# Kernel tuning notes

Hardware: AMD Instinct MI355X
Metric: run time of the kernel (lower is better)

The kernel has to match this reference:

```python
import jax, jax.numpy as jnp
import numpy as np

N_AE = 512
N_DE = 256
N = 100000
NUM_SEG = 1024
EPS = 1e-5


def setup_inputs() -> dict:
    key = jax.random.key(0)
    ks = jax.random.split(key, 20)
    d_in1 = 2 * N_AE + N_DE  # 1280
    inp = {
        "x": jax.random.normal(ks[0], (N, 2 * N_AE), dtype=jnp.float32),
        "dist_feat": jax.random.normal(ks[1], (N, N_DE), dtype=jnp.float32),
        "atom_idx": jax.random.randint(ks[2], (N,), 0, 100, dtype=jnp.int32),
        "ele_idx": jax.random.randint(ks[3], (N,), 0, NUM_SEG, dtype=jnp.int32),
        # layer 1 params
        "l1_w": jax.random.normal(ks[4], (d_in1, N_AE), dtype=jnp.float32) * (1.0 / np.sqrt(d_in1)),
        "l1_b": jnp.zeros((N_AE,), dtype=jnp.float32),
        "l1_g": jnp.ones((N_AE,), dtype=jnp.float32),
        "l1_be": jnp.zeros((N_AE,), dtype=jnp.float32),
        # layer 2 params (same input width: 2*n_ae + n_de)
        "l2_w": jax.random.normal(ks[5], (d_in1, N_AE), dtype=jnp.float32) * (1.0 / np.sqrt(d_in1)),
        "l2_b": jnp.zeros((N_AE,), dtype=jnp.float32),
        "l2_g": jnp.ones((N_AE,), dtype=jnp.float32),
        "l2_be": jnp.zeros((N_AE,), dtype=jnp.float32),
        # final fc + bn
        "f_w": jax.random.normal(ks[6], (2 * N_AE, N_AE), dtype=jnp.float32) * (1.0 / np.sqrt(2 * N_AE)),
        "f_b": jnp.zeros((N_AE,), dtype=jnp.float32),
        "f_g": jnp.ones((N_AE,), dtype=jnp.float32),
        "f_be": jnp.zeros((N_AE,), dtype=jnp.float32),
    }
    return inp


def _bn(h, gamma, beta):
    # BatchNorm1d in training mode: batch stats, biased variance
    m = jnp.mean(h, axis=0)
    v = jnp.mean(jnp.square(h - m), axis=0)
    return gamma * (h - m) * jax.lax.rsqrt(v + EPS) + beta


def _dist_layer(x_cat, ele_idx, w, b, gamma, beta):
    h = jax.nn.relu(_bn(x_cat @ w + b, gamma, beta))  # [N, n_ae]
    sums = jax.ops.segment_sum(h, ele_idx, num_segments=NUM_SEG)  # [S, n_ae]
    cnt = jax.ops.segment_sum(jnp.ones((h.shape[0],), h.dtype), ele_idx, num_segments=NUM_SEG)
    mean = sums / jnp.maximum(cnt, 1.0)[:, None]
    return jnp.concatenate([h, mean[ele_idx]], axis=1)  # [N, 2*n_ae]


def reference(x, dist_feat, atom_idx, ele_idx,
              l1_w, l1_b, l1_g, l1_be,
              l2_w, l2_b, l2_g, l2_be,
              f_w, f_b, f_g, f_be):
    h = _dist_layer(jnp.concatenate([x, dist_feat], axis=1), ele_idx, l1_w, l1_b, l1_g, l1_be)
    h = _dist_layer(jnp.concatenate([h, dist_feat], axis=1), ele_idx, l2_w, l2_b, l2_g, l2_be)
    out = jax.nn.relu(_bn(h @ f_w + f_b, f_g, f_be))  # [N, n_ae]
    return out
```

## Files before the change

kernel.cpp:

```cpp
#include <hip/hip_runtime.h>
#include <stdint.h>
#include <stdio.h>

#define NOUT 512
#define NSEG 1024

typedef unsigned short u16;
typedef __attribute__((ext_vector_type(4))) float f32x4;
typedef __attribute__((ext_vector_type(8))) short s16x8;
typedef __attribute__((ext_vector_type(4))) unsigned short u16x4;

__device__ __forceinline__ u16 f2b(float f) {
  union { float f; uint32_t u; } v; v.f = f;
  uint32_t r = v.u + 0x7FFFu + ((v.u >> 16) & 1u);
  return (u16)(r >> 16);
}
__device__ __forceinline__ float b2f(u16 b) {
  union { uint32_t u; float f; } v; v.u = ((uint32_t)b) << 16;
  return v.f;
}

typedef __attribute__((address_space(1))) const void GAS;
typedef __attribute__((address_space(3))) void LAS;
__device__ __forceinline__ void llds16(const void* g, void* l) {
  __builtin_amdgcn_global_load_lds((GAS*)g, (LAS*)l, 16, 0, 0);
}

__global__ void k_cast2(const float* __restrict__ x, u16* __restrict__ xb, long n4x,
                        const float* __restrict__ d, u16* __restrict__ db, long n4d) {
  long i0 = blockIdx.x * (long)blockDim.x + threadIdx.x;
  long stride = (long)gridDim.x * blockDim.x;
  for (long i = i0; i < n4x; i += stride) {
    float4 v = reinterpret_cast<const float4*>(x)[i];
    u16x4 o;
    o.x = f2b(v.x); o.y = f2b(v.y); o.z = f2b(v.z); o.w = f2b(v.w);
    reinterpret_cast<u16x4*>(xb)[i] = o;
  }
  for (long i = i0; i < n4d; i += stride) {
    float4 v = reinterpret_cast<const float4*>(d)[i];
    u16x4 o;
    o.x = f2b(v.x); o.y = f2b(v.y); o.z = f2b(v.z); o.w = f2b(v.w);
    reinterpret_cast<u16x4*>(db)[i] = o;
  }
}

__global__ void k_wtcastT3(const float* __restrict__ w0, u16* __restrict__ o0,
                           const float* __restrict__ w1, u16* __restrict__ o1,
                           const float* __restrict__ w2, u16* __restrict__ o2) {
  __shared__ float tile[32][33];
  int z = blockIdx.z;
  const float* w = z == 0 ? w0 : (z == 1 ? w1 : w2);
  u16* out = z == 0 ? o0 : (z == 1 ? o1 : o2);
  int K = z == 2 ? 1024 : 1280;
  int k0 = blockIdx.x * 32, c0 = blockIdx.y * 32;
  if (k0 >= K) return;
  int t = threadIdx.x;
  int rr = t >> 5, cc = t & 31;
#pragma unroll
  for (int p = 0; p < 4; ++p)
    tile[p * 8 + rr][cc] = w[(long)(k0 + p * 8 + rr) * NOUT + c0 + cc];
  __syncthreads();
#pragma unroll
  for (int p = 0; p < 4; ++p)
    out[(long)(c0 + p * 8 + rr) * K + k0 + cc] = f2b(tile[cc][p * 8 + rr]);
}

__global__ void k_hist(const int* __restrict__ ele, int* __restrict__ cnt, int N) {
  int i = blockIdx.x * blockDim.x + threadIdx.x;
  int stride = gridDim.x * blockDim.x;
  for (; i < N; i += stride) atomicAdd(&cnt[ele[i]], 1);
}

__global__ void k_scan(const int* __restrict__ cnt, int* __restrict__ off) {
  __shared__ int tmp[NSEG];
  int t = threadIdx.x;
  tmp[t] = cnt[t];
  __syncthreads();
  for (int o = 1; o < NSEG; o <<= 1) {
    int add = (t >= o) ? tmp[t - o] : 0;
    __syncthreads();
    tmp[t] += add;
    __syncthreads();
  }
  off[t] = tmp[t] - cnt[t];
}

__global__ void k_scatter(const int* __restrict__ ele, const int* __restrict__ off,
                          int* __restrict__ fill, int* __restrict__ rows, int N) {
  int i = blockIdx.x * blockDim.x + threadIdx.x;
  int stride = gridDim.x * blockDim.x;
  for (; i < N; i += stride) {
    int e = ele[i];
    int p = atomicAdd(&fill[e], 1);
    rows[off[e] + p] = i;
  }
}

__global__ void k_bnseg(const u16* __restrict__ hp, u16* __restrict__ h, u16* __restrict__ mean,
                        const float* __restrict__ stats, const float* __restrict__ g,
                        const float* __restrict__ be, float invM,
                        const int* __restrict__ off, const int* __restrict__ cnt,
                        const int* __restrict__ rows) {
  int s = blockIdx.x;
  int c0 = 2 * threadIdx.x;
  int n = cnt[s], o = off[s];
  float m0 = stats[c0] * invM, m1 = stats[c0 + 1] * invM;
  float v0 = stats[NOUT + c0] * invM - m0 * m0;
  float v1 = stats[NOUT + c0 + 1] * invM - m1 * m1;
  float a0 = g[c0] * rsqrtf(v0 + 1e-5f);
  float a1 = g[c0 + 1] * rsqrtf(v1 + 1e-5f);
  float cc0 = be[c0] - a0 * m0;
  float cc1 = be[c0 + 1] - a1 * m1;
  float s0 = 0.f, s1 = 0.f;
#pragma unroll 2
  for (int j = 0; j < n; ++j) {
    int r = rows[o + j];
    uint32_t v = *reinterpret_cast<const uint32_t*>(&hp[(long)r * NOUT + c0]);
    float h0 = fmaxf(a0 * b2f((u16)(v & 0xffff)) + cc0, 0.f);
    float h1 = fmaxf(a1 * b2f((u16)(v >> 16)) + cc1, 0.f);
    s0 += h0; s1 += h1;
    *reinterpret_cast<uint32_t*>(&h[(long)r * NOUT + c0]) =
        ((uint32_t)f2b(h1) << 16) | (uint32_t)f2b(h0);
  }
  float inv = 1.f / fmaxf((float)n, 1.f);
  *reinterpret_cast<uint32_t*>(&mean[(long)s * NOUT + c0]) =
      ((uint32_t)f2b(s1 * inv) << 16) | (uint32_t)f2b(s0 * inv);
}

__global__ void k_final(const u16* __restrict__ hp, float* __restrict__ out,
                        const float* __restrict__ stats, const float* __restrict__ g,
                        const float* __restrict__ be, float invM, long n4) {
  __shared__ float sA[NOUT], sC[NOUT];
  for (int c = threadIdx.x; c < NOUT; c += blockDim.x) {
    float m = stats[c] * invM;
    float v = stats[NOUT + c] * invM - m * m;
    float a = g[c] * rsqrtf(v + 1e-5f);
    sA[c] = a;
    sC[c] = be[c] - a * m;
  }
  __syncthreads();
  long i = blockIdx.x * (long)blockDim.x + threadIdx.x;
  long stride = (long)gridDim.x * blockDim.x;
  for (; i < n4; i += stride) {
    u16x4 v = reinterpret_cast<const u16x4*>(hp)[i];
    int c0 = (int)((i * 4) & (NOUT - 1));
    float4 a = *reinterpret_cast<const float4*>(&sA[c0]);
    float4 c = *reinterpret_cast<const float4*>(&sC[c0]);
    float4 o;
    o.x = fmaxf(a.x * b2f(v.x) + c.x, 0.f);
    o.y = fmaxf(a.y * b2f(v.y) + c.y, 0.f);
    o.z = fmaxf(a.z * b2f(v.z) + c.z, 0.f);
    o.w = fmaxf(a.w * b2f(v.w) + c.w, 0.f);
    reinterpret_cast<float4*>(out)[i] = o;
  }
}

template <int K, int E0, int E0B, int BSKIP>
__global__ __launch_bounds__(256, 4) void k_gemm(
    const u16* p0, const u16* p1, int w0, int w1, int g0, int g1,
    const int* __restrict__ ele,
    const u16* __restrict__ wbt, int ldb,
    const float* __restrict__ tab, int addtab,
    u16* __restrict__ outp, float* __restrict__ outf, int wf32,
    float* __restrict__ csum, float* __restrict__ csq, int dostats,
    int M) {
  __shared__ __align__(16) u16 As[2 * 4096];
  __shared__ __align__(16) u16 Bs[2 * 4096];

  int nwg = gridDim.x;
  int orig = blockIdx.x;
  int q = nwg >> 3, r8 = nwg & 7;
  int xcd = orig & 7, loc = orig >> 3;
  int bid = (xcd < r8 ? xcd * (q + 1) : r8 * (q + 1) + (xcd - r8) * q) + loc;
  int mt = bid >> 2, ct = bid & 3;
  int brow = mt * 128, bcol = ct * 128;

  int tid = (int)threadIdx.x;
  int lane = tid & 63;
  int wid = tid >> 6;
  int wr = wid >> 1, wc = wid & 1;
  int l15 = lane & 15, kg = lane >> 4;

  int srow = tid >> 2;
  int soct = ((tid & 3) ^ ((srow >> 1) & 3)) * 8;

  int gr0 = brow + srow, gr1 = gr0 + 64;
  int gr0c = gr0 < M ? gr0 : M - 1;
  int gr1c = gr1 < M ? gr1 : M - 1;
  int el0 = (g0 | g1) ? ele[gr0c] : 0, el1 = (g0 | g1) ? ele[gr1c] : 0;

  const u16* a00 = p0 + (long)(g0 ? el0 : gr0c) * w0 + soct;
  const u16* a01 = p1 + (long)(g1 ? el0 : gr0c) * w1 + soct - E0;
  const u16* a10 = p0 + (long)(g0 ? el1 : gr1c) * w0 + soct;
  const u16* a11 = p1 + (long)(g1 ? el1 : gr1c) * w1 + soct - E0;

  const u16* b0p = wbt + (long)(bcol + srow) * ldb + soct;
  const u16* b1p = wbt + (long)(bcol + srow + 64) * ldb + soct;

  int xoct = (kg ^ ((l15 >> 1) & 3)) * 8;
  int aro = (wr * 64 + l15) * 32 + xoct;
  int bro = (wc * 64 + l15) * 32 + xoct;

  f32x4 acc[4][4];
#pragma unroll
  for (int m = 0; m < 4; ++m)
#pragma unroll
    for (int n = 0; n < 4; ++n)
#pragma unroll
      for (int j = 0; j < 4; ++j) acc[m][n][j] = 0.f;

  constexpr int KT = K >> 5;
  int dst = wid * 512;

  auto stage = [&](int tt, int buf) {
    int k0 = tt << 5;
    const u16* sa0 = k0 < E0 ? a00 : a01;
    const u16* sa1 = k0 < E0 ? a10 : a11;
    int bo = k0 + (k0 >= E0B ? BSKIP : 0);
    int ab = buf * 4096 + dst;
    llds16(sa0 + k0, &As[ab]);
    llds16(sa1 + k0, &As[ab + 2048]);
    llds16(b0p + bo, &Bs[ab]);
    llds16(b1p + bo, &Bs[ab + 2048]);
  };

  stage(0, 0);
  __syncthreads();

#pragma unroll
  for (int t = 0; t < KT; ++t) {
    int cur = t & 1;
    if (t + 1 < KT) stage(t + 1, cur ^ 1);
    __builtin_amdgcn_sched_barrier(0);
    const u16* Ab = &As[cur * 4096];
    const u16* Bb = &Bs[cur * 4096];
    s16x8 af[4], bf[4];
#pragma unroll
    for (int m = 0; m < 4; ++m)
      af[m] = *reinterpret_cast<const s16x8*>(&Ab[m * 512 + aro]);
#pragma unroll
    for (int n = 0; n < 4; ++n)
      bf[n] = *reinterpret_cast<const s16x8*>(&Bb[n * 512 + bro]);
#pragma unroll
    for (int m = 0; m < 4; ++m)
#pragma unroll
      for (int n = 0; n < 4; ++n)
        acc[m][n] = __builtin_amdgcn_mfma_f32_16x16x32_bf16(af[m], bf[n], acc[m][n], 0, 0, 0);
    __syncthreads();
  }

  float sums[4] = {0.f, 0.f, 0.f, 0.f}, sqs[4] = {0.f, 0.f, 0.f, 0.f};
#pragma unroll
  for (int m = 0; m < 4; ++m) {
    int row0 = brow + wr * 64 + m * 16 + kg * 4;
#pragma unroll
    for (int j = 0; j < 4; ++j) {
      int r = row0 + j;
      if (r < M) {
        long rb = (long)r * NOUT;
        long tb = addtab ? (long)ele[r] * NOUT : 0;
#pragma unroll
        for (int n = 0; n < 4; ++n) {
          int col = bcol + wc * 64 + n * 16 + l15;
          float v = acc[m][n][j];
          if (addtab) v += tab[tb + col];
          if (wf32) outf[rb + col] = v;
          else outp[rb + col] = f2b(v);
          sums[n] += v;
          sqs[n] += v * v;
        }
      }
    }
  }
  if (dostats) {
#pragma unroll
    for (int n = 0; n < 4; ++n) {
      sums[n] += __shfl_xor(sums[n], 16);
      sums[n] += __shfl_xor(sums[n], 32);
      sqs[n] += __shfl_xor(sqs[n], 16);
      sqs[n] += __shfl_xor(sqs[n], 32);
    }
    if (kg == 0) {
#pragma unroll
      for (int n = 0; n < 4; ++n) {
        int col = bcol + wc * 64 + n * 16 + l15;
        atomicAdd(&csum[col], sums[n]);
        atomicAdd(&csq[col], sqs[n]);
      }
    }
  }
}

extern "C" void kernel_launch(void* const* d_in, const int* in_sizes, int n_in,
                              void* d_out, int out_size, void* d_ws, size_t ws_size,
                              hipStream_t stream) {
  const float* x    = (const float*)d_in[0];
  const float* dist = (const float*)d_in[1];
  const int* ele    = (const int*)d_in[3];
  const float* l1w  = (const float*)d_in[4];
  const float* l1g  = (const float*)d_in[6];
  const float* l1be = (const float*)d_in[7];
  const float* l2w  = (const float*)d_in[8];
  const float* l2g  = (const float*)d_in[10];
  const float* l2be = (const float*)d_in[11];
  const float* fw   = (const float*)d_in[12];
  const float* fg   = (const float*)d_in[14];
  const float* fbe  = (const float*)d_in[15];

  int N = in_sizes[0] / 1024;
  float* out = (float*)d_out;
  u16* xbf = (u16*)d_out;

  int MT = (N + 127) / 128;

  char* w = (char*)d_ws;
  auto alloc = [&](size_t bytes) {
    char* p = w;
    w += (bytes + 255) & ~(size_t)255;
    return p;
  };
  u16* dist_bf = (u16*)alloc((size_t)N * 256 * 2);
  u16* hp      = (u16*)alloc((size_t)N * NOUT * 2);
  u16* h       = (u16*)alloc((size_t)N * NOUT * 2);
  u16* mean    = (u16*)alloc((size_t)NSEG * NOUT * 2);
  u16* w1bt    = (u16*)alloc((size_t)NOUT * 1280 * 2);
  u16* w2bt    = (u16*)alloc((size_t)NOUT * 1280 * 2);
  u16* fbt     = (u16*)alloc((size_t)NOUT * 1024 * 2);
  float* mc2   = (float*)alloc((size_t)NSEG * NOUT * 4);
  float* mc3   = (float*)alloc((size_t)NSEG * NOUT * 4);
  char* zz0    = w;
  int* seg_cnt = (int*)alloc(NSEG * 4);
  int* seg_fill = (int*)alloc(NSEG * 4);
  float* stats1 = (float*)alloc(NOUT * 2 * 4);
  float* stats2 = (float*)alloc(NOUT * 2 * 4);
  float* stats3 = (float*)alloc(NOUT * 2 * 4);
  size_t zzlen = (size_t)(w - zz0);
  int* seg_off = (int*)alloc(NSEG * 4);
  int* rows    = (int*)alloc((size_t)N * 4);

  size_t need = (size_t)(w - (char*)d_ws);
  if (need > ws_size) {
    fprintf(stderr, "kernel_launch: ws too small: need %zu have %zu\n", need, ws_size);
    return;
  }

  long n4x = (long)N * 1024 / 4;
  long n4d = (long)N * 256 / 4;
  long n4h = (long)N * NOUT / 4;
  int gemmGrid = MT * 4;
  int mcGrid = (NSEG / 128) * 4;
  float invM = 1.0f / (float)N;

  k_cast2<<<4096, 256, 0, stream>>>(x, xbf, n4x, dist, dist_bf, n4d);
  dim3 wtg(1280 / 32, NOUT / 32, 3);
  k_wtcastT3<<<wtg, 256, 0, stream>>>(l1w, w1bt, l2w, w2bt, fw, fbt);
  hipMemsetAsync(zz0, 0, zzlen, stream);

  k_hist<<<512, 256, 0, stream>>>(ele, seg_cnt, N);
  k_scan<<<1, NSEG, 0, stream>>>(seg_cnt, seg_off);
  k_scatter<<<512, 256, 0, stream>>>(ele, seg_off, seg_fill, rows, N);

  k_gemm<1280, 1024, 1280, 0><<<gemmGrid, 256, 0, stream>>>(
      xbf, dist_bf, 1024, 256, 0, 0, ele, w1bt, 1280, mc2, 0,
      hp, mc2, 0, stats1, stats1 + NOUT, 1, N);
  k_bnseg<<<NSEG, 256, 0, stream>>>(hp, h, mean, stats1, l1g, l1be, invM,
                                    seg_off, seg_cnt, rows);

  k_gemm<512, 512, 512, 0><<<mcGrid, 256, 0, stream>>>(
      mean, mean, 512, 512, 0, 0, ele, w2bt + 512, 1280, mc2, 0,
      hp, mc2, 1, stats2, stats2 + NOUT, 0, NSEG);
  k_gemm<768, 512, 512, 512><<<gemmGrid, 256, 0, stream>>>(
      h, dist_bf, 512, 256, 0, 0, ele, w2bt, 1280, mc2, 1,
      hp, mc2, 0, stats2, stats2 + NOUT, 1, N);
  k_bnseg<<<NSEG, 256, 0, stream>>>(hp, h, mean, stats2, l2g, l2be, invM,
                                    seg_off, seg_cnt, rows);

  k_gemm<512, 512, 512, 0><<<mcGrid, 256, 0, stream>>>(
      mean, mean, 512, 512, 0, 0, ele, fbt + 512, 1024, mc3, 0,
      hp, mc3, 1, stats3, stats3 + NOUT, 0, NSEG);
  k_gemm<512, 512, 512, 0><<<gemmGrid, 256, 0, stream>>>(
      h, h, 512, 512, 0, 0, ele, fbt, 1024, mc3, 1,
      hp, mc3, 0, stats3, stats3 + NOUT, 1, N);
  k_final<<<4096, 256, 0, stream>>>(hp, out, stats3, fg, fbe, invM, n4h);
}
```

Measured before the change: 908.6 us.

## Enlarge GEMM row tile from 128 to 192 with per-wave loading

The GEMM block tile grows from 128x128 to 192x128, so each wave computes a 96x64 sub-tile with 6x4 MFMA accumulators. Global-to-LDS staging is reorganised so each wave loads three A row-groups and two B row-groups, and the launch bound is lowered to 3 blocks per CU to make room for the extra registers and LDS. The aim is more reuse of each B fragment per LDS load and fewer blocks overall. The cost is lower occupancy, more register pressure, and more wasted rows on the small 1024-row mean GEMM.

Result: slower. 1.023 ms (+12.6%).

```diff
diff --git a/kernel.cpp b/kernel.cpp
--- a/kernel.cpp
+++ b/kernel.cpp
@@ -156,7 +156,7 @@
 }
 
 template <int K, int E0, int E0B, int BSKIP>
-__global__ __launch_bounds__(256, 4) void k_gemm(
+__global__ __launch_bounds__(256, 3) void k_gemm(
     const u16* p0, const u16* p1, int w0, int w1, int g0, int g1,
     const int* __restrict__ ele,
     const u16* __restrict__ wbt, int ldb,
@@ -164,7 +164,7 @@
     u16* __restrict__ outp, float* __restrict__ outf, int wf32,
     float* __restrict__ csum, float* __restrict__ csq, int dostats,
     int M) {
-  __shared__ __align__(16) u16 As[2 * 4096];
+  __shared__ __align__(16) u16 As[2 * 6144];
   __shared__ __align__(16) u16 Bs[2 * 4096];
 
   int nwg = gridDim.x;
@@ -173,7 +173,7 @@
   int xcd = orig & 7, loc = orig >> 3;
   int bid = (xcd < r8 ? xcd * (q + 1) : r8 * (q + 1) + (xcd - r8) * q) + loc;
   int mt = bid >> 2, ct = bid & 3;
-  int brow = mt * 128, bcol = ct * 128;
+  int brow = mt * 192, bcol = ct * 128;
 
   int tid = (int)threadIdx.x;
   int lane = tid & 63;
@@ -181,47 +181,52 @@
   int wr = wid >> 1, wc = wid & 1;
   int l15 = lane & 15, kg = lane >> 4;
 
-  int srow = tid >> 2;
-  int soct = ((tid & 3) ^ ((srow >> 1) & 3)) * 8;
-
-  int gr0 = brow + srow, gr1 = gr0 + 64;
-  int gr0c = gr0 < M ? gr0 : M - 1;
-  int gr1c = gr1 < M ? gr1 : M - 1;
-  int el0 = (g0 | g1) ? ele[gr0c] : 0, el1 = (g0 | g1) ? ele[gr1c] : 0;
-
-  const u16* a00 = p0 + (long)(g0 ? el0 : gr0c) * w0 + soct;
-  const u16* a01 = p1 + (long)(g1 ? el0 : gr0c) * w1 + soct - E0;
-  const u16* a10 = p0 + (long)(g0 ? el1 : gr1c) * w0 + soct;
-  const u16* a11 = p1 + (long)(g1 ? el1 : gr1c) * w1 + soct - E0;
-
-  const u16* b0p = wbt + (long)(bcol + srow) * ldb + soct;
-  const u16* b1p = wbt + (long)(bcol + srow + 64) * ldb + soct;
+  int lrow = lane >> 2;
+  int lsoct = ((lane & 3) ^ ((lane >> 3) & 3)) * 8;
+
+  const u16 *a0p[3], *a1p[3];
+#pragma unroll
+  for (int i = 0; i < 3; ++i) {
+    int gr = brow + 16 * (wid * 3 + i) + lrow;
+    if (gr >= M) gr = M - 1;
+    int e = (g0 | g1) ? ele[gr] : 0;
+    a0p[i] = p0 + (long)(g0 ? e : gr) * w0 + lsoct;
+    a1p[i] = p1 + (long)(g1 ? e : gr) * w1 + lsoct - E0;
+  }
+  const u16* bp[2];
+#pragma unroll
+  for (int i = 0; i < 2; ++i)
+    bp[i] = wbt + (long)(bcol + 16 * (wid * 2 + i) + lrow) * ldb + lsoct;
 
   int xoct = (kg ^ ((l15 >> 1) & 3)) * 8;
-  int aro = (wr * 64 + l15) * 32 + xoct;
+  int aro = (wr * 96 + l15) * 32 + xoct;
   int bro = (wc * 64 + l15) * 32 + xoct;
 
-  f32x4 acc[4][4];
-#pragma unroll
-  for (int m = 0; m < 4; ++m)
+  f32x4 acc[6][4];
+#pragma unroll
+  for (int m = 0; m < 6; ++m)
 #pragma unroll
     for (int n = 0; n < 4; ++n)
 #pragma unroll
       for (int j = 0; j < 4; ++j) acc[m][n][j] = 0.f;
 
   constexpr int KT = K >> 5;
-  int dst = wid * 512;
 
   auto stage = [&](int tt, int buf) {
     int k0 = tt << 5;
-    const u16* sa0 = k0 < E0 ? a00 : a01;
-    const u16* sa1 = k0 < E0 ? a10 : a11;
     int bo = k0 + (k0 >= E0B ? BSKIP : 0);
-    int ab = buf * 4096 + dst;
-    llds16(sa0 + k0, &As[ab]);
-    llds16(sa1 + k0, &As[ab + 2048]);
-    llds16(b0p + bo, &Bs[ab]);
-    llds16(b1p + bo, &Bs[ab + 2048]);
+    if (k0 < E0) {
+#pragma unroll
+      for (int i = 0; i < 3; ++i)
+        llds16(a0p[i] + k0, &As[buf * 6144 + (wid * 3 + i) * 512]);
+    } else {
+#pragma unroll
+      for (int i = 0; i < 3; ++i)
+        llds16(a1p[i] + k0, &As[buf * 6144 + (wid * 3 + i) * 512]);
+    }
+#pragma unroll
+    for (int i = 0; i < 2; ++i)
+      llds16(bp[i] + bo, &Bs[buf * 4096 + (wid * 2 + i) * 512]);
   };
 
   stage(0, 0);
@@ -232,17 +237,17 @@
     int cur = t & 1;
     if (t + 1 < KT) stage(t + 1, cur ^ 1);
     __builtin_amdgcn_sched_barrier(0);
-    const u16* Ab = &As[cur * 4096];
+    const u16* Ab = &As[cur * 6144];
     const u16* Bb = &Bs[cur * 4096];
-    s16x8 af[4], bf[4];
-#pragma unroll
-    for (int m = 0; m < 4; ++m)
+    s16x8 af[6], bf[4];
+#pragma unroll
+    for (int m = 0; m < 6; ++m)
       af[m] = *reinterpret_cast<const s16x8*>(&Ab[m * 512 + aro]);
 #pragma unroll
     for (int n = 0; n < 4; ++n)
       bf[n] = *reinterpret_cast<const s16x8*>(&Bb[n * 512 + bro]);
 #pragma unroll
-    for (int m = 0; m < 4; ++m)
+    for (int m = 0; m < 6; ++m)
 #pragma unroll
       for (int n = 0; n < 4; ++n)
         acc[m][n] = __builtin_amdgcn_mfma_f32_16x16x32_bf16(af[m], bf[n], acc[m][n], 0, 0, 0);
@@ -251,8 +256,8 @@
 
   float sums[4] = {0.f, 0.f, 0.f, 0.f}, sqs[4] = {0.f, 0.f, 0.f, 0.f};
 #pragma unroll
-  for (int m = 0; m < 4; ++m) {
-    int row0 = brow + wr * 64 + m * 16 + kg * 4;
+  for (int m = 0; m < 6; ++m) {
+    int row0 = brow + wr * 96 + m * 16 + kg * 4;
 #pragma unroll
     for (int j = 0; j < 4; ++j) {
       int r = row0 + j;
@@ -311,7 +316,8 @@
   float* out = (float*)d_out;
   u16* xbf = (u16*)d_out;
 
-  int MT = (N + 127) / 128;
+  int MT = (N + 191) / 192;
+  int mcMT = (NSEG + 191) / 192;
 
   char* w = (char*)d_ws;
   auto alloc = [&](size_t bytes) {
@@ -348,7 +354,7 @@
   long n4d = (long)N * 256 / 4;
   long n4h = (long)N * NOUT / 4;
   int gemmGrid = MT * 4;
-  int mcGrid = (NSEG / 128) * 4;
+  int mcGrid = mcMT * 4;
   float invM = 1.0f / (float)N;
 
   k_cast2<<<4096, 256, 0, stream>>>(x, xbf, n4x, dist, dist_bf, n4d);
```
